# Optimization experiments

Hardware: AMD Instinct MI355X
Metric: run time of the kernel (lower is better)

Reference implementation:

```python
import jax, jax.numpy as jnp
import numpy as np

IN_C = 128
OUT_C = 128
HEADS = 8
HEAD_DIM = OUT_C // HEADS
N_NODES = 4096
N_EDGES = 131072


def setup_inputs() -> dict:
    key = jax.random.key(0)
    ks = jax.random.split(key, 10)
    s_in = 1.0 / np.sqrt(IN_C)
    s_out = 1.0 / np.sqrt(OUT_C)
    return {
        "x": jax.random.normal(ks[0], (N_NODES, IN_C), dtype=jnp.float32),
        "edge_index": jax.random.randint(ks[1], (2, N_EDGES), 0, N_NODES, dtype=jnp.int64),
        "Wq": jax.random.uniform(ks[2], (IN_C, OUT_C), jnp.float32, -s_in, s_in),
        "bq": jnp.zeros((OUT_C,), jnp.float32),
        "Wk": jax.random.uniform(ks[3], (IN_C, OUT_C), jnp.float32, -s_in, s_in),
        "bk": jnp.zeros((OUT_C,), jnp.float32),
        "Wv": jax.random.uniform(ks[4], (IN_C, OUT_C), jnp.float32, -s_in, s_in),
        "bv": jnp.zeros((OUT_C,), jnp.float32),
        "Wo": jax.random.uniform(ks[5], (OUT_C, OUT_C), jnp.float32, -s_out, s_out),
        "bo": jnp.zeros((OUT_C,), jnp.float32),
    }


def reference(x, edge_index, Wq, bq, Wk, bk, Wv, bv, Wo, bo):
    n = x.shape[0]
    Q = (x @ Wq + bq).reshape(n, HEADS, HEAD_DIM)
    K = (x @ Wk + bk).reshape(n, HEADS, HEAD_DIM)
    V = (x @ Wv + bv).reshape(n, HEADS, HEAD_DIM)
    # dense scores [n, m, h], matching the original module's einsum
    scores = jnp.einsum('nhd,mhd->nmh', Q, K) / np.sqrt(HEAD_DIM).astype(np.float32)
    ei = jnp.clip(edge_index, 0, n - 1)
    mask = jnp.zeros((n, n), dtype=bool).at[ei[0], ei[1]].set(True)
    scores = jnp.where(mask[:, :, None], scores, -jnp.inf)
    attention = jax.nn.softmax(scores, axis=1)
    # rows (along m) that were all -inf give NaN -> replace with 1/n, as in torch
    attention = jnp.nan_to_num(attention, nan=1.0 / n)
    out = jnp.einsum('nmh,mhd->nhd', attention, V).reshape(n, OUT_C)
    return out @ Wo + bo
```

## Files before the change

### kernel.cpp

```cpp
#include <hip/hip_runtime.h>
#include <math.h>

#define NN 4096
#define NE 131072
#define C 128
#define NH 8
#define HD 16
#define RCAP 96
#define UCAP 64

__device__ __forceinline__ float dot16(const float* __restrict__ q, const float* __restrict__ kp) {
    const float4* k4 = reinterpret_cast<const float4*>(kp);
    const float4 k0 = k4[0], k1 = k4[1], k2 = k4[2], k3 = k4[3];
    return q[0]*k0.x + q[1]*k0.y + q[2]*k0.z + q[3]*k0.w
         + q[4]*k1.x + q[5]*k1.y + q[6]*k1.z + q[7]*k1.w
         + q[8]*k2.x + q[9]*k2.y + q[10]*k2.z + q[11]*k2.w
         + q[12]*k3.x + q[13]*k3.y + q[14]*k3.z + q[15]*k3.w;
}

__global__ __launch_bounds__(256) void qkv_kernel(
    const float* __restrict__ x,
    const float* __restrict__ Wq, const float* __restrict__ bq,
    const float* __restrict__ Wk, const float* __restrict__ bk,
    const float* __restrict__ Wv, const float* __restrict__ bv,
    float* __restrict__ Q, float* __restrict__ K, float* __restrict__ V,
    int* __restrict__ deg)
{
    if (threadIdx.x < 16) deg[blockIdx.x * 16 + threadIdx.x] = 0;

    __shared__ float xs[16][C];
    const int n0 = blockIdx.x * 16;
    for (int i = threadIdx.x; i < 16 * C; i += 256)
        xs[i >> 7][i & 127] = x[n0 * C + i];
    __syncthreads();

    const int c = threadIdx.x & 127;
    const int half = threadIdx.x >> 7;
    float aq[8], ak[8], av[8];
    #pragma unroll
    for (int j = 0; j < 8; j++) { aq[j] = 0.f; ak[j] = 0.f; av[j] = 0.f; }

    for (int k = 0; k < C; k++) {
        const float wq = Wq[k * C + c];
        const float wk = Wk[k * C + c];
        const float wv = Wv[k * C + c];
        #pragma unroll
        for (int j = 0; j < 8; j++) {
            const float xv = xs[half * 8 + j][k];
            aq[j] = fmaf(xv, wq, aq[j]);
            ak[j] = fmaf(xv, wk, ak[j]);
            av[j] = fmaf(xv, wv, av[j]);
        }
    }
    const float bqv = bq[c], bkv = bk[c], bvv = bv[c];
    #pragma unroll
    for (int j = 0; j < 8; j++) {
        const int n = n0 + half * 8 + j;
        Q[n * C + c] = aq[j] + bqv;
        K[n * C + c] = ak[j] + bkv;
        V[n * C + c] = av[j] + bvv;
    }
}

__global__ __launch_bounds__(256) void scatter_kernel(
    const int* __restrict__ ei, int* __restrict__ deg,
    unsigned short* __restrict__ nbr)
{
    const int e = blockIdx.x * 256 + threadIdx.x;
    int src = ei[e];
    int dst = ei[NE + e];
    src = src < 0 ? 0 : (src > NN - 1 ? NN - 1 : src);
    dst = dst < 0 ? 0 : (dst > NN - 1 ? NN - 1 : dst);
    const int p = atomicAdd(&deg[src], 1);
    if (p < RCAP) nbr[src * RCAP + p] = (unsigned short)dst;
}

__global__ __launch_bounds__(256, 4) void attn_proj_kernel(
    const float* __restrict__ Q, const float* __restrict__ K,
    const float* __restrict__ V, const int* __restrict__ deg,
    const unsigned short* __restrict__ nbr, const float* __restrict__ Wo,
    const float* __restrict__ bo, float* __restrict__ out)
{
    __shared__ unsigned int bitmap[8][128];
    __shared__ unsigned short lst[8][UCAP];
    __shared__ int cnt[8];
    __shared__ float row[8][C];

    const int tid = threadIdx.x;
    const int w = tid >> 6;
    const int lane = tid & 63;
    const int base = blockIdx.x * 8;
    const int h = lane & 7;
    const int sub = lane >> 3;

    for (int i = tid; i < 8 * 128; i += 256) (&bitmap[0][0])[i] = 0u;
    if (tid < 8) cnt[tid] = 0;
    __syncthreads();

    for (int rep = 0; rep < 2; rep++) {
        const int nl = w * 2 + rep;
        const int n = base + nl;
        const int rdeg = min(deg[n], RCAP);

        for (int i = lane; i < rdeg; i += 64) {
            const int dst = nbr[n * RCAP + i];
            const unsigned int bit = 1u << (dst & 31);
            const unsigned int old = atomicOr(&bitmap[nl][dst >> 5], bit);
            if (!(old & bit)) {
                const int p = atomicAdd(&cnt[nl], 1);
                if (p < UCAP) lst[nl][p] = (unsigned short)dst;
            }
        }
        asm volatile("s_waitcnt lgkmcnt(0)" ::: "memory");
        const int dg = min(cnt[nl], UCAP);

        if (dg == 0) {
            for (int d = lane; d < C; d += 64) {
                float s2 = 0.f;
                for (int m = 0; m < NN; m++) s2 += V[m * C + d];
                row[nl][d] = s2 * (1.f / (float)NN);
            }
            continue;
        }

        float qh[16];
        {
            const float4* qp = reinterpret_cast<const float4*>(Q + n * C + h * HD);
            const float4 q0 = qp[0], q1 = qp[1], q2 = qp[2], q3 = qp[3];
            qh[0]=q0.x; qh[1]=q0.y; qh[2]=q0.z; qh[3]=q0.w;
            qh[4]=q1.x; qh[5]=q1.y; qh[6]=q1.z; qh[7]=q1.w;
            qh[8]=q2.x; qh[9]=q2.y; qh[10]=q2.z; qh[11]=q2.w;
            qh[12]=q3.x; qh[13]=q3.y; qh[14]=q3.z; qh[15]=q3.w;
        }
        int id[8];
        #pragma unroll
        for (int j = 0; j < 8; j++) {
            const int i = sub + 8 * j;
            id[j] = (i < dg) ? lst[nl][i] : -1;
        }
        float s[8];
        #pragma unroll
        for (int j = 0; j < 8; j++)
            s[j] = (id[j] >= 0) ? dot16(qh, K + id[j] * C + h * HD) * 0.25f : -INFINITY;
        float M = s[0];
        #pragma unroll
        for (int j = 1; j < 8; j++) M = fmaxf(M, s[j]);
        #pragma unroll
        for (int o = 8; o < 64; o <<= 1) M = fmaxf(M, __shfl_xor(M, o, 64));
        float p[8], ss = 0.f;
        #pragma unroll
        for (int j = 0; j < 8; j++) {
            p[j] = (id[j] >= 0) ? __expf(s[j] - M) : 0.f;
            ss += p[j];
        }
        #pragma unroll
        for (int o = 8; o < 64; o <<= 1) ss += __shfl_xor(ss, o, 64);
        const float inv = 1.f / ss;
        #pragma unroll
        for (int j = 0; j < 8; j++) p[j] *= inv;
        float acc[16];
        #pragma unroll
        for (int d = 0; d < 16; d++) acc[d] = 0.f;
        #pragma unroll
        for (int j = 0; j < 8; j++) {
            if (id[j] >= 0) {
                const float4* v4 = reinterpret_cast<const float4*>(V + id[j] * C + h * HD);
                const float4 v0 = v4[0], v1 = v4[1], v2 = v4[2], v3 = v4[3];
                acc[0]  = fmaf(p[j], v0.x, acc[0]);  acc[1]  = fmaf(p[j], v0.y, acc[1]);
                acc[2]  = fmaf(p[j], v0.z, acc[2]);  acc[3]  = fmaf(p[j], v0.w, acc[3]);
                acc[4]  = fmaf(p[j], v1.x, acc[4]);  acc[5]  = fmaf(p[j], v1.y, acc[5]);
                acc[6]  = fmaf(p[j], v1.z, acc[6]);  acc[7]  = fmaf(p[j], v1.w, acc[7]);
                acc[8]  = fmaf(p[j], v2.x, acc[8]);  acc[9]  = fmaf(p[j], v2.y, acc[9]);
                acc[10] = fmaf(p[j], v2.z, acc[10]); acc[11] = fmaf(p[j], v2.w, acc[11]);
                acc[12] = fmaf(p[j], v3.x, acc[12]); acc[13] = fmaf(p[j], v3.y, acc[13]);
                acc[14] = fmaf(p[j], v3.z, acc[14]); acc[15] = fmaf(p[j], v3.w, acc[15]);
            }
        }
        #pragma unroll
        for (int o = 8; o < 64; o <<= 1) {
            #pragma unroll
            for (int d = 0; d < 16; d++)
                acc[d] += __shfl_xor(acc[d], o, 64);
        }
        if (sub == 0) {
            float4* rp = reinterpret_cast<float4*>(&row[nl][h * HD]);
            rp[0] = make_float4(acc[0],  acc[1],  acc[2],  acc[3]);
            rp[1] = make_float4(acc[4],  acc[5],  acc[6],  acc[7]);
            rp[2] = make_float4(acc[8],  acc[9],  acc[10], acc[11]);
            rp[3] = make_float4(acc[12], acc[13], acc[14], acc[15]);
        }
    }
    __syncthreads();

    const int c = tid & 127;
    const int g = tid >> 7;
    float a0 = 0.f, a1 = 0.f, a2 = 0.f, a3 = 0.f;
    #pragma unroll 4
    for (int k = 0; k < C; k++) {
        const float wo = Wo[k * C + c];
        a0 = fmaf(row[g][k],     wo, a0);
        a1 = fmaf(row[g + 2][k], wo, a1);
        a2 = fmaf(row[g + 4][k], wo, a2);
        a3 = fmaf(row[g + 6][k], wo, a3);
    }
    const float bov = bo[c];
    out[(base + g) * C + c]     = a0 + bov;
    out[(base + g + 2) * C + c] = a1 + bov;
    out[(base + g + 4) * C + c] = a2 + bov;
    out[(base + g + 6) * C + c] = a3 + bov;
}

extern "C" void kernel_launch(void* const* d_in, const int* in_sizes, int n_in,
                              void* d_out, int out_size, void* d_ws, size_t ws_size,
                              hipStream_t stream)
{
    const float* x  = (const float*)d_in[0];
    const int*   ei = (const int*)d_in[1];
    const float* Wq = (const float*)d_in[2];
    const float* bq = (const float*)d_in[3];
    const float* Wk = (const float*)d_in[4];
    const float* bk = (const float*)d_in[5];
    const float* Wv = (const float*)d_in[6];
    const float* bv = (const float*)d_in[7];
    const float* Wo = (const float*)d_in[8];
    const float* bo = (const float*)d_in[9];
    float* out = (float*)d_out;

    char* ws = (char*)d_ws;
    const size_t MB2 = 1u << 21;
    float*          Q   = (float*)(ws);
    float*          K   = (float*)(ws + MB2);
    float*          V   = (float*)(ws + 2 * MB2);
    int*            deg = (int*)(ws + 3 * MB2);
    unsigned short* nbr = (unsigned short*)(ws + 3 * MB2 + (1 << 16));

    qkv_kernel<<<NN / 16, 256, 0, stream>>>(x, Wq, bq, Wk, bk, Wv, bv, Q, K, V, deg);
    scatter_kernel<<<NE / 256, 256, 0, stream>>>(ei, deg, nbr);
    attn_proj_kernel<<<NN / 8, 256, 0, stream>>>(Q, K, V, deg, nbr, Wo, bo, out);
}
```

Before: 60.22 us.

## Use online softmax with early V loads and widen QKV projection blocks

The attention kernel now issues K and V gathers together in two batches of four neighbours and uses an online-softmax rescale, so V loads no longer wait behind the max and sum reductions. This reduces the serial latency chain per node, but it holds more live registers, and the launch bound drops to 2 blocks per SM. The QKV kernel moves to 512 threads with 4 rows per thread, a single float4 load of x, and an unrolled k loop, to raise parallelism and memory-level concurrency.

```diff
diff --git a/kernel.cpp b/kernel.cpp
--- a/kernel.cpp
+++ b/kernel.cpp
@@ -18,7 +18,7 @@
          + q[12]*k3.x + q[13]*k3.y + q[14]*k3.z + q[15]*k3.w;
 }
 
-__global__ __launch_bounds__(256) void qkv_kernel(
+__global__ __launch_bounds__(512) void qkv_kernel(
     const float* __restrict__ x,
     const float* __restrict__ Wq, const float* __restrict__ bq,
     const float* __restrict__ Wk, const float* __restrict__ bk,
@@ -26,27 +26,29 @@
     float* __restrict__ Q, float* __restrict__ K, float* __restrict__ V,
     int* __restrict__ deg)
 {
-    if (threadIdx.x < 16) deg[blockIdx.x * 16 + threadIdx.x] = 0;
+    const int tid = threadIdx.x;
+    if (tid < 16) deg[blockIdx.x * 16 + tid] = 0;
 
     __shared__ float xs[16][C];
     const int n0 = blockIdx.x * 16;
-    for (int i = threadIdx.x; i < 16 * C; i += 256)
-        xs[i >> 7][i & 127] = x[n0 * C + i];
+    reinterpret_cast<float4*>(&xs[0][0])[tid] =
+        reinterpret_cast<const float4*>(x + n0 * C)[tid];
     __syncthreads();
 
-    const int c = threadIdx.x & 127;
-    const int half = threadIdx.x >> 7;
-    float aq[8], ak[8], av[8];
+    const int c = tid & 127;
+    const int q = tid >> 7;
+    float aq[4], ak[4], av[4];
     #pragma unroll
-    for (int j = 0; j < 8; j++) { aq[j] = 0.f; ak[j] = 0.f; av[j] = 0.f; }
-
+    for (int j = 0; j < 4; j++) { aq[j] = 0.f; ak[j] = 0.f; av[j] = 0.f; }
+
+    #pragma unroll 4
     for (int k = 0; k < C; k++) {
         const float wq = Wq[k * C + c];
         const float wk = Wk[k * C + c];
         const float wv = Wv[k * C + c];
         #pragma unroll
-        for (int j = 0; j < 8; j++) {
-            const float xv = xs[half * 8 + j][k];
+        for (int j = 0; j < 4; j++) {
+            const float xv = xs[q + 4 * j][k];
             aq[j] = fmaf(xv, wq, aq[j]);
             ak[j] = fmaf(xv, wk, ak[j]);
             av[j] = fmaf(xv, wv, av[j]);
@@ -54,8 +56,8 @@
     }
     const float bqv = bq[c], bkv = bk[c], bvv = bv[c];
     #pragma unroll
-    for (int j = 0; j < 8; j++) {
-        const int n = n0 + half * 8 + j;
+    for (int j = 0; j < 4; j++) {
+        const int n = n0 + q + 4 * j;
         Q[n * C + c] = aq[j] + bqv;
         K[n * C + c] = ak[j] + bkv;
         V[n * C + c] = av[j] + bvv;
@@ -75,7 +77,7 @@
     if (p < RCAP) nbr[src * RCAP + p] = (unsigned short)dst;
 }
 
-__global__ __launch_bounds__(256, 4) void attn_proj_kernel(
+__global__ __launch_bounds__(256, 2) void attn_proj_kernel(
     const float* __restrict__ Q, const float* __restrict__ K,
     const float* __restrict__ V, const int* __restrict__ deg,
     const unsigned short* __restrict__ nbr, const float* __restrict__ Wo,
@@ -136,58 +138,88 @@
         #pragma unroll
         for (int j = 0; j < 8; j++) {
             const int i = sub + 8 * j;
-            id[j] = (i < dg) ? lst[nl][i] : -1;
-        }
+            id[j] = (i < dg) ? (int)lst[nl][i] : -1;
+        }
+
+        float acc[16];
+        #pragma unroll
+        for (int d = 0; d < 16; d++) acc[d] = 0.f;
         float s[8];
-        #pragma unroll
-        for (int j = 0; j < 8; j++)
-            s[j] = (id[j] >= 0) ? dot16(qh, K + id[j] * C + h * HD) * 0.25f : -INFINITY;
-        float M = s[0];
-        #pragma unroll
-        for (int j = 1; j < 8; j++) M = fmaxf(M, s[j]);
+
+        float4 va[4][4];
+        #pragma unroll
+        for (int j = 0; j < 4; j++) {
+            const int idx = id[j] >= 0 ? id[j] : 0;
+            s[j] = (id[j] >= 0) ? dot16(qh, K + idx * C + h * HD) * 0.25f : -INFINITY;
+            const float4* vp = reinterpret_cast<const float4*>(V + idx * C + h * HD);
+            va[j][0] = vp[0]; va[j][1] = vp[1]; va[j][2] = vp[2]; va[j][3] = vp[3];
+        }
+        const float mA = fmaxf(fmaxf(s[0], s[1]), fmaxf(s[2], s[3]));
+        float ssum = 0.f;
+        #pragma unroll
+        for (int j = 0; j < 4; j++) {
+            const float p = (id[j] >= 0) ? __expf(s[j] - mA) : 0.f;
+            ssum += p;
+            acc[0]  = fmaf(p, va[j][0].x, acc[0]);  acc[1]  = fmaf(p, va[j][0].y, acc[1]);
+            acc[2]  = fmaf(p, va[j][0].z, acc[2]);  acc[3]  = fmaf(p, va[j][0].w, acc[3]);
+            acc[4]  = fmaf(p, va[j][1].x, acc[4]);  acc[5]  = fmaf(p, va[j][1].y, acc[5]);
+            acc[6]  = fmaf(p, va[j][1].z, acc[6]);  acc[7]  = fmaf(p, va[j][1].w, acc[7]);
+            acc[8]  = fmaf(p, va[j][2].x, acc[8]);  acc[9]  = fmaf(p, va[j][2].y, acc[9]);
+            acc[10] = fmaf(p, va[j][2].z, acc[10]); acc[11] = fmaf(p, va[j][2].w, acc[11]);
+            acc[12] = fmaf(p, va[j][3].x, acc[12]); acc[13] = fmaf(p, va[j][3].y, acc[13]);
+            acc[14] = fmaf(p, va[j][3].z, acc[14]); acc[15] = fmaf(p, va[j][3].w, acc[15]);
+        }
+
+        float4 vb[4][4];
+        #pragma unroll
+        for (int j = 4; j < 8; j++) {
+            const int idx = id[j] >= 0 ? id[j] : 0;
+            s[j] = (id[j] >= 0) ? dot16(qh, K + idx * C + h * HD) * 0.25f : -INFINITY;
+            const float4* vp = reinterpret_cast<const float4*>(V + idx * C + h * HD);
+            vb[j-4][0] = vp[0]; vb[j-4][1] = vp[1]; vb[j-4][2] = vp[2]; vb[j-4][3] = vp[3];
+        }
+        const float mB = fmaxf(fmaxf(s[4], s[5]), fmaxf(s[6], s[7]));
+        const float ml = fmaxf(mA, mB);
+        const float fA = (ml == -INFINITY) ? 0.f : __expf(mA - ml);
+        ssum *= fA;
+        #pragma unroll
+        for (int d = 0; d < 16; d++) acc[d] *= fA;
+        #pragma unroll
+        for (int j = 4; j < 8; j++) {
+            const float p = (id[j] >= 0) ? __expf(s[j] - ml) : 0.f;
+            ssum += p;
+            acc[0]  = fmaf(p, vb[j-4][0].x, acc[0]);  acc[1]  = fmaf(p, vb[j-4][0].y, acc[1]);
+            acc[2]  = fmaf(p, vb[j-4][0].z, acc[2]);  acc[3]  = fmaf(p, vb[j-4][0].w, acc[3]);
+            acc[4]  = fmaf(p, vb[j-4][1].x, acc[4]);  acc[5]  = fmaf(p, vb[j-4][1].y, acc[5]);
+            acc[6]  = fmaf(p, vb[j-4][1].z, acc[6]);  acc[7]  = fmaf(p, vb[j-4][1].w, acc[7]);
+            acc[8]  = fmaf(p, vb[j-4][2].x, acc[8]);  acc[9]  = fmaf(p, vb[j-4][2].y, acc[9]);
+            acc[10] = fmaf(p, vb[j-4][2].z, acc[10]); acc[11] = fmaf(p, vb[j-4][2].w, acc[11]);
+            acc[12] = fmaf(p, vb[j-4][3].x, acc[12]); acc[13] = fmaf(p, vb[j-4][3].y, acc[13]);
+            acc[14] = fmaf(p, vb[j-4][3].z, acc[14]); acc[15] = fmaf(p, vb[j-4][3].w, acc[15]);
+        }
+
+        float M = ml;
         #pragma unroll
         for (int o = 8; o < 64; o <<= 1) M = fmaxf(M, __shfl_xor(M, o, 64));
-        float p[8], ss = 0.f;
-        #pragma unroll
-        for (int j = 0; j < 8; j++) {
-            p[j] = (id[j] >= 0) ? __expf(s[j] - M) : 0.f;
-            ss += p[j];
-        }
-        #pragma unroll
-        for (int o = 8; o < 64; o <<= 1) ss += __shfl_xor(ss, o, 64);
-        const float inv = 1.f / ss;
-        #pragma unroll
-        for (int j = 0; j < 8; j++) p[j] *= inv;
-        float acc[16];
-        #pragma unroll
-        for (int d = 0; d < 16; d++) acc[d] = 0.f;
-        #pragma unroll
-        for (int j = 0; j < 8; j++) {
-            if (id[j] >= 0) {
-                const float4* v4 = reinterpret_cast<const float4*>(V + id[j] * C + h * HD);
-                const float4 v0 = v4[0], v1 = v4[1], v2 = v4[2], v3 = v4[3];
-                acc[0]  = fmaf(p[j], v0.x, acc[0]);  acc[1]  = fmaf(p[j], v0.y, acc[1]);
-                acc[2]  = fmaf(p[j], v0.z, acc[2]);  acc[3]  = fmaf(p[j], v0.w, acc[3]);
-                acc[4]  = fmaf(p[j], v1.x, acc[4]);  acc[5]  = fmaf(p[j], v1.y, acc[5]);
-                acc[6]  = fmaf(p[j], v1.z, acc[6]);  acc[7]  = fmaf(p[j], v1.w, acc[7]);
-                acc[8]  = fmaf(p[j], v2.x, acc[8]);  acc[9]  = fmaf(p[j], v2.y, acc[9]);
-                acc[10] = fmaf(p[j], v2.z, acc[10]); acc[11] = fmaf(p[j], v2.w, acc[11]);
-                acc[12] = fmaf(p[j], v3.x, acc[12]); acc[13] = fmaf(p[j], v3.y, acc[13]);
-                acc[14] = fmaf(p[j], v3.z, acc[14]); acc[15] = fmaf(p[j], v3.w, acc[15]);
-            }
-        }
+        const float f = (ml == -INFINITY) ? 0.f : __expf(ml - M);
+        ssum *= f;
+        #pragma unroll
+        for (int d = 0; d < 16; d++) acc[d] *= f;
+        #pragma unroll
+        for (int o = 8; o < 64; o <<= 1) ssum += __shfl_xor(ssum, o, 64);
         #pragma unroll
         for (int o = 8; o < 64; o <<= 1) {
             #pragma unroll
             for (int d = 0; d < 16; d++)
                 acc[d] += __shfl_xor(acc[d], o, 64);
         }
+        const float inv = 1.f / ssum;
         if (sub == 0) {
             float4* rp = reinterpret_cast<float4*>(&row[nl][h * HD]);
-            rp[0] = make_float4(acc[0],  acc[1],  acc[2],  acc[3]);
-            rp[1] = make_float4(acc[4],  acc[5],  acc[6],  acc[7]);
-            rp[2] = make_float4(acc[8],  acc[9],  acc[10], acc[11]);
-            rp[3] = make_float4(acc[12], acc[13], acc[14], acc[15]);
+            rp[0] = make_float4(acc[0]*inv,  acc[1]*inv,  acc[2]*inv,  acc[3]*inv);
+            rp[1] = make_float4(acc[4]*inv,  acc[5]*inv,  acc[6]*inv,  acc[7]*inv);
+            rp[2] = make_float4(acc[8]*inv,  acc[9]*inv,  acc[10]*inv, acc[11]*inv);
+            rp[3] = make_float4(acc[12]*inv, acc[13]*inv, acc[14]*inv, acc[15]*inv);
         }
     }
     __syncthreads();
@@ -234,7 +266,7 @@
     int*            deg = (int*)(ws + 3 * MB2);
     unsigned short* nbr = (unsigned short*)(ws + 3 * MB2 + (1 << 16));
 
-    qkv_kernel<<<NN / 16, 256, 0, stream>>>(x, Wq, bq, Wk, bk, Wv, bv, Q, K, V, deg);
+    qkv_kernel<<<NN / 16, 512, 0, stream>>>(x, Wq, bq, Wk, bk, Wv, bv, Q, K, V, deg);
     scatter_kernel<<<NE / 256, 256, 0, stream>>>(ei, deg, nbr);
     attn_proj_kernel<<<NN / 8, 256, 0, stream>>>(Q, K, V, deg, nbr, Wo, bo, out);
 }
```

After: 59.30 us. Within noise of the previous version (-1.5%).
